# Kernel tuning notes

Measured on AMD Instinct MI355X. Metric: run time of the kernel, lower is better.

The kernel has to match this reference:

```python
import jax, jax.numpy as jnp
import numpy as np

D_MODEL, H, DK, DV = 1024, 16, 64, 64
B, NQ, NK = 4, 1024, 1024
LN_EPS = 1e-5


def setup_inputs() -> dict:
    key = jax.random.key(0)
    ks = jax.random.split(key, 16)
    xavier = lambda k, i, o: jax.random.uniform(k, (i, o), jnp.float32,
                                                -np.sqrt(6.0 / (i + o)), np.sqrt(6.0 / (i + o)))
    return {
        "queries": jax.random.normal(ks[0], (B, NQ, D_MODEL), jnp.float32),
        "keys": jax.random.normal(ks[1], (B, NK, D_MODEL), jnp.float32),
        "values": jax.random.normal(ks[2], (B, NK, D_MODEL), jnp.float32),
        "geometry": jax.random.uniform(ks[3], (B, H, NQ, NK), jnp.float32),
        "attention_mask": jax.random.bernoulli(ks[4], 0.1, (B, H, NQ, NK)),
        "Wq": xavier(ks[5], D_MODEL, H * DK), "bq": jnp.zeros((H * DK,), jnp.float32),
        "Wk": xavier(ks[6], D_MODEL, H * DK), "bk": jnp.zeros((H * DK,), jnp.float32),
        "Wv": xavier(ks[7], D_MODEL, H * DV), "bv": jnp.zeros((H * DV,), jnp.float32),
        "Wo": xavier(ks[8], H * DV, D_MODEL), "bo": jnp.zeros((D_MODEL,), jnp.float32),
        "ln_gamma": jnp.ones((D_MODEL,), jnp.float32),
        "ln_beta": jnp.zeros((D_MODEL,), jnp.float32),
    }


def reference(queries, keys, values, geometry, attention_mask,
              Wq, bq, Wk, bk, Wv, bv, Wo, bo, ln_gamma, ln_beta):
    b, nq, _ = queries.shape
    nk = keys.shape[1]
    # QKV projections -> (b, h, n, d)
    q = (queries @ Wq + bq).reshape(b, nq, H, DK).transpose(0, 2, 1, 3)
    k = (keys @ Wk + bk).reshape(b, nk, H, DK).transpose(0, 2, 1, 3)
    v = (values @ Wv + bv).reshape(b, nk, H, DV).transpose(0, 2, 1, 3)
    att = jnp.einsum('bhqd,bhkd->bhqk', q, k) / np.sqrt(DK).astype(np.float32)
    att = jnp.where(attention_mask, -jnp.inf, att)
    # inline geometry log-bias before softmax
    w = jnp.log(jnp.clip(geometry, 1e-6)) + att
    w = jax.nn.softmax(w, axis=-1)  # dropout is identity in eval
    out = jnp.einsum('bhqk,bhkd->bqhd', w, v).reshape(b, nq, H * DV)
    out = out @ Wo + bo
    # residual + LayerNorm
    x = queries + out  # dropout identity in eval
    mu = jnp.mean(x, axis=-1, keepdims=True)
    var = jnp.mean((x - mu) ** 2, axis=-1, keepdims=True)
    return (x - mu) * jax.lax.rsqrt(var + LN_EPS) * ln_gamma + ln_beta
```

## Files before the change

kernel.cpp:

```cpp
#include <hip/hip_runtime.h>
#include <hip/hip_bf16.h>

typedef unsigned short u16;
typedef unsigned char u8;
typedef unsigned long long u64;
typedef __bf16 bf16x8 __attribute__((ext_vector_type(8)));
typedef float f32x4 __attribute__((ext_vector_type(4)));

#define AS1 __attribute__((address_space(1)))
#define AS3 __attribute__((address_space(3)))
#define GLL16(gp, lp) __builtin_amdgcn_global_load_lds((AS1 const unsigned int*)(gp), (AS3 unsigned int*)(lp), 16, 0, 0)
#define NTL4(p) __builtin_nontemporal_load((const f32x4*)(p))

__device__ __forceinline__ u16 f2bf(float f) {
    unsigned u = __builtin_bit_cast(unsigned, f);
    unsigned r = u + 0x7FFFu + ((u >> 16) & 1u);
    return (u16)(r >> 16);
}

__global__ __launch_bounds__(256) void prep_kernel(
    const float* __restrict__ q, const float* __restrict__ k, const float* __restrict__ v,
    u16* __restrict__ xq, u16* __restrict__ xk, u16* __restrict__ xv,
    const float* __restrict__ W0, const float* __restrict__ W1,
    const float* __restrict__ W2, const float* __restrict__ W3,
    u16* __restrict__ T0, u16* __restrict__ T1, u16* __restrict__ T2, u16* __restrict__ T3) {
    const int gb = blockIdx.x, tid = threadIdx.x;
    if (gb < 1024) {
        const int n4 = 4 * 1024 * 1024 / 4;
        const int stride = 1024 * 256;
        for (int i = gb * 256 + tid; i < n4; i += stride) {
            float4 a = ((const float4*)q)[i];
            float4 b = ((const float4*)k)[i];
            float4 c = ((const float4*)v)[i];
            ((ushort4*)xq)[i] = make_ushort4(f2bf(a.x), f2bf(a.y), f2bf(a.z), f2bf(a.w));
            ((ushort4*)xk)[i] = make_ushort4(f2bf(b.x), f2bf(b.y), f2bf(b.z), f2bf(b.w));
            ((ushort4*)xv)[i] = make_ushort4(f2bf(c.x), f2bf(c.y), f2bf(c.z), f2bf(c.w));
        }
    } else {
        __shared__ float t[64][65];
        const int idx = gb - 1024;
        const int bz = idx >> 8, by = (idx >> 4) & 15, bx = idx & 15;
        const float* W = (bz == 0) ? W0 : (bz == 1) ? W1 : (bz == 2) ? W2 : W3;
        u16* T = (bz == 0) ? T0 : (bz == 1) ? T1 : (bz == 2) ? T2 : T3;
        const int n0 = bx * 64, k0 = by * 64;
        const int tx = tid & 63, ty = tid >> 6;
        for (int j = ty; j < 64; j += 4) t[j][tx] = W[(size_t)(k0 + j) * 1024 + n0 + tx];
        __syncthreads();
        for (int j = ty; j < 64; j += 4) T[(size_t)(n0 + j) * 1024 + k0 + tx] = f2bf(t[tx][j]);
    }
}

#define MN_LOOP(PRED)                                                     \
    for (int row = wave; row < 65536; row += nw) {                        \
        size_t base = (size_t)row * 1024;                                 \
        u64 myw = 0;                                                      \
        _Pragma("unroll")                                                 \
        for (int kb = 0; kb < 16; ++kb) {                                 \
            size_t gi = base + kb * 64 + lane;                            \
            bool p = (PRED);                                              \
            u64 w = __ballot(p);                                          \
            if (lane == kb) myw = w;                                      \
        }                                                                 \
        if (lane < 16) MB[(size_t)row * 16 + lane] = myw;                 \
    }

__global__ __launch_bounds__(256) void masknorm_kernel(const void* __restrict__ mp,
                                                       u64* __restrict__ MB) {
    __shared__ int s_cnt1, s_big;
    if (threadIdx.x == 0) { s_cnt1 = 0; s_big = 0; }
    __syncthreads();
    {
        const unsigned char* m8 = (const unsigned char*)mp;
        int c1 = 0, bg = 0;
        for (int i = threadIdx.x; i < 16384; i += 256) {
            unsigned char vv = m8[i];
            if (vv) {
                if ((i & 3) == 1) c1++;
                if (vv > 1) bg++;
            }
        }
        atomicAdd(&s_cnt1, c1);
        atomicAdd(&s_big, bg);
    }
    __syncthreads();
    const int flag = (s_big == 0) ? (s_cnt1 ? 0 : 1) : (s_cnt1 ? 3 : 2);

    const int lane = threadIdx.x & 63;
    const int wave = blockIdx.x * 4 + (threadIdx.x >> 6);
    const int nw = gridDim.x * 4;
    if (flag == 0) {
        const unsigned char* m8 = (const unsigned char*)mp;
        MN_LOOP(m8[gi] != 0)
    } else if (flag == 1) {
        const int* m32 = (const int*)mp;
        MN_LOOP(m32[gi] != 0)
    } else if (flag == 2) {
        const unsigned* mf = (const unsigned*)mp;
        MN_LOOP((mf[gi] << 1) != 0)
    } else {
        const u16* mb = (const u16*)mp;
        MN_LOOP((mb[gi] & 0x7FFF) != 0)
    }
}

__device__ __forceinline__ void gemm_core(const u16* __restrict__ A, const u16* __restrict__ Bt,
                                          u16* sA, u16* sB, f32x4 (&acc)[4][4],
                                          int tid, int bm, int bn) {
    const int lane = tid & 63, wid = tid >> 6;
    const int wr = wid >> 1, wc = wid & 1;
    const int l15 = lane & 15, l4 = lane >> 4;
    const int srow = tid >> 2, sslot = tid & 3;
    const int soff = (sslot ^ ((srow >> 1) & 3)) * 8;
    const u16* aSrc = A + (size_t)(bm * 128 + srow) * 1024 + soff;
    const u16* bSrc = Bt + (size_t)(bn * 128 + srow) * 1024 + soff;
    u16* const dA0 = sA + wid * 512;
    u16* const dA1 = sA + 2048 + wid * 512;
    u16* const dB0 = sB + wid * 512;
    u16* const dB1 = sB + 2048 + wid * 512;

#define GSTAGE(BUF, T)                                                  \
    do {                                                                \
        GLL16(aSrc + (T) * 32, dA0 + (BUF) * 4096);                     \
        GLL16(aSrc + 65536 + (T) * 32, dA1 + (BUF) * 4096);             \
        GLL16(bSrc + (T) * 32, dB0 + (BUF) * 4096);                     \
        GLL16(bSrc + 65536 + (T) * 32, dB1 + (BUF) * 4096);             \
    } while (0)

#define GCOMPUTE(BUF)                                                             \
    do {                                                                          \
        bf16x8 af[4], bfv[4];                                                     \
        _Pragma("unroll")                                                         \
        for (int m = 0; m < 4; ++m) {                                             \
            const int rr = wr * 64 + m * 16 + l15;                                \
            af[m] = *(const bf16x8*)(sA + (BUF) * 4096 + rr * 32 +                \
                                     ((l4 ^ ((rr >> 1) & 3)) * 8));               \
        }                                                                         \
        _Pragma("unroll")                                                         \
        for (int n = 0; n < 4; ++n) {                                             \
            const int rr = wc * 64 + n * 16 + l15;                                \
            bfv[n] = *(const bf16x8*)(sB + (BUF) * 4096 + rr * 32 +               \
                                      ((l4 ^ ((rr >> 1) & 3)) * 8));              \
        }                                                                         \
        _Pragma("unroll")                                                         \
        for (int m = 0; m < 4; ++m)                                               \
            _Pragma("unroll")                                                     \
            for (int n = 0; n < 4; ++n)                                           \
                acc[m][n] = __builtin_amdgcn_mfma_f32_16x16x32_bf16(af[m], bfv[n], acc[m][n], 0, 0, 0); \
    } while (0)

#define GBODY(T, BUF, NBUF, WSTR)                                       \
    do {                                                                \
        if ((T) + 2 < 32) {                                             \
            GSTAGE(NBUF, (T) + 2);                                      \
            __builtin_amdgcn_sched_barrier(0);                          \
        }                                                               \
        GCOMPUTE(BUF);                                                  \
        if ((T) + 1 < 32) {                                             \
            asm volatile(WSTR ::: "memory");                            \
            __builtin_amdgcn_sched_barrier(0);                          \
            __builtin_amdgcn_s_barrier();                               \
            __builtin_amdgcn_sched_barrier(0);                          \
        }                                                               \
    } while (0)

    GSTAGE(0, 0);
    GSTAGE(1, 1);
    __builtin_amdgcn_sched_barrier(0);
    asm volatile("s_waitcnt vmcnt(4)" ::: "memory");
    __builtin_amdgcn_sched_barrier(0);
    __builtin_amdgcn_s_barrier();
    __builtin_amdgcn_sched_barrier(0);

    for (int it = 0; it < 10; ++it) {
        const int t0 = it * 3;
        GBODY(t0 + 0, 0, 2, "s_waitcnt vmcnt(4)");
        GBODY(t0 + 1, 1, 0, "s_waitcnt vmcnt(4)");
        GBODY(t0 + 2, 2, 1, "s_waitcnt vmcnt(4)");
    }
    GBODY(30, 0, 2, "s_waitcnt vmcnt(0)");
    GBODY(31, 1, 0, "s_waitcnt vmcnt(0)");
#undef GBODY
#undef GCOMPUTE
#undef GSTAGE
}

__global__ __launch_bounds__(256, 3) void qkv_gemm(
    const u16* __restrict__ XQ, const u16* __restrict__ XK, const u16* __restrict__ XV,
    const u16* __restrict__ WQT, const u16* __restrict__ WKT, const u16* __restrict__ WVT,
    const float* __restrict__ bq, const float* __restrict__ bk, const float* __restrict__ bv,
    u16* __restrict__ QS, u16* __restrict__ KS, u16* __restrict__ VT) {
    __shared__ __align__(16) u16 smem[24576];
    const int z = blockIdx.z;
    const u16* A  = (z == 0) ? XQ : (z == 1) ? XK : XV;
    const u16* Bt = (z == 0) ? WQT : (z == 1) ? WKT : WVT;
    const float* bias = (z == 0) ? bq : (z == 1) ? bk : bv;
    const int tid = threadIdx.x, lane = tid & 63, wid = tid >> 6;
    const int bm = blockIdx.x * 4 + (blockIdx.y >> 3);
    const int bn = blockIdx.y & 7;
    const int wr = wid >> 1, wc = wid & 1;
    const int l15 = lane & 15, l4 = lane >> 4;

    f32x4 acc[4][4] = {};
    gemm_core(A, Bt, smem, smem + 12288, acc, tid, bm, bn);

    if (z == 2) {
        __syncthreads();
        u16* tl = smem;
#pragma unroll
        for (int n = 0; n < 4; ++n) {
            const int cl = wc * 64 + n * 16 + l15;
            const float bv_ = bias[bn * 128 + cl];
#pragma unroll
            for (int m = 0; m < 4; ++m)
#pragma unroll
                for (int j = 0; j < 4; ++j) {
                    const int rl = wr * 64 + m * 16 + l4 * 4 + j;
                    tl[cl * 132 + rl] = f2bf(acc[m][n][j] + bv_);
                }
        }
        __syncthreads();
        const int bb = bm >> 3, k0 = (bm & 7) * 128;
#pragma unroll
        for (int i = 0; i < 8; ++i) {
            const int idx = i * 256 + tid;
            const int row = idx >> 4, col16 = idx & 15;
            const int cg = bn * 128 + row;
            const int hh = cg >> 6, dd = cg & 63;
            bf16x8 v = *(const bf16x8*)(tl + row * 132 + col16 * 8);
            *(bf16x8*)(VT + ((size_t)((bb * 16 + hh) * 64 + dd)) * 1024 + k0 + col16 * 8) = v;
        }
    } else {
        u16* outp = (z == 0) ? QS : KS;
        const float scale = (z == 0) ? 0.125f : 1.0f;
#pragma unroll
        for (int n = 0; n < 4; ++n) {
            const int c = bn * 128 + wc * 64 + n * 16 + l15;
            const float bv_ = bias[c];
#pragma unroll
            for (int m = 0; m < 4; ++m)
#pragma unroll
                for (int j = 0; j < 4; ++j) {
                    const int r = bm * 128 + wr * 64 + m * 16 + l4 * 4 + j;
                    outp[(size_t)r * 1024 + c] = f2bf((acc[m][n][j] + bv_) * scale);
                }
        }
    }
}

__global__ __launch_bounds__(256, 3) void gemm_out(
    const u16* __restrict__ A, const u16* __restrict__ Bt, const float* __restrict__ bias,
    float* __restrict__ outp, const float* __restrict__ resid) {
    __shared__ __align__(16) u16 smem[24576];
    const int tid = threadIdx.x, lane = tid & 63, wid = tid >> 6;
    const int bm = blockIdx.x * 4 + (blockIdx.y >> 3);
    const int bn = blockIdx.y & 7;
    const int wr = wid >> 1, wc = wid & 1;
    const int l15 = lane & 15, l4 = lane >> 4;

    f32x4 acc[4][4] = {};
    gemm_core(A, Bt, smem, smem + 12288, acc, tid, bm, bn);

#pragma unroll
    for (int n = 0; n < 4; ++n) {
        const int c = bn * 128 + wc * 64 + n * 16 + l15;
        const float bv = bias[c];
#pragma unroll
        for (int m = 0; m < 4; ++m)
#pragma unroll
            for (int j = 0; j < 4; ++j) {
                const int r = bm * 128 + wr * 64 + m * 16 + l4 * 4 + j;
                outp[(size_t)r * 1024 + c] = acc[m][n][j] + bv + resid[(size_t)r * 1024 + c];
            }
    }
}

__global__ __launch_bounds__(256, 3) void attn_kernel(
    const u16* __restrict__ Qs, const u16* __restrict__ Ks, const u16* __restrict__ Vt,
    const float* __restrict__ geom, const u64* __restrict__ MBw,
    u16* __restrict__ AO) {
    __shared__ __align__(16) u16 lds[20480];

    const int g = blockIdx.x;
    const int tt = (g & 7) * 128 + (g >> 3);
    const int qb = tt & 15;
    const int bhid = tt >> 4;
    const int b = bhid >> 4, h = bhid & 15;
    const int q0 = qb * 64;

    const int tid = threadIdx.x, lane = tid & 63, wid = tid >> 6;
    const int l15 = lane & 15, l4 = lane >> 4;
    const int qrow = q0 + wid * 16;
    const size_t bh = (size_t)bhid;

    const u16* qp = Qs + (size_t)(b * 1024 + qrow + l15) * 1024 + h * 64 + l4 * 8;
    bf16x8 aq0 = *(const bf16x8*)qp;
    bf16x8 aq1 = *(const bf16x8*)(qp + 32);

    const int r0 = tid >> 3, s0 = tid & 7;
    const int r1 = 32 + r0;
    const int kgr0 = (r0 & 15) * 4 + (r0 >> 4);
    const int kgr1 = (r1 & 15) * 4 + (r1 >> 4);
    const u16* ksrc0 = Ks + (size_t)(b * 1024 + kgr0) * 1024 + h * 64 + ((s0 ^ (r0 & 7)) * 8);
    const u16* ksrc1 = Ks + (size_t)(b * 1024 + kgr1) * 1024 + h * 64 + ((s0 ^ (r1 & 7)) * 8);
    const u16* vsrc0 = Vt + (bh * 64 + r0) * 1024 + ((s0 ^ (r0 & 7)) * 8);
    const u16* vsrc1 = Vt + (bh * 64 + r1) * 1024 + ((s0 ^ (r1 & 7)) * 8);
    u16* const KD = lds + wid * 512;
    u16* const VD = lds + 8192 + wid * 512;
    u16* const pw = lds + 16384 + wid * 1024;

    const float* gbase = geom + (bh * 1024 + qrow + l4 * 4) * 1024 + l15 * 4;
    const u8* mbase8 = (const u8*)MBw + (size_t)(bh * 1024 + qrow + l4 * 4) * 128 + (l15 >> 1);
    const int nsh = (l15 & 1) * 4;

    f32x4 o[4] = {};
    float m_run[4], l_run[4];
#pragma unroll
    for (int j = 0; j < 4; ++j) { m_run[j] = -1e30f; l_run[j] = 0.f; }

    f32x4 gpA[4], gpB[4];
    unsigned mkA[4], mkB[4];

    GLL16(ksrc0, KD);
    GLL16(ksrc1, KD + 2048);
    GLL16(vsrc0, VD);
    GLL16(vsrc1, VD + 2048);
    __builtin_amdgcn_sched_barrier(0);
#pragma unroll
    for (int j = 0; j < 4; ++j) {
        gpA[j] = NTL4(gbase + j * 1024);
        mkA[j] = __builtin_nontemporal_load(mbase8 + j * 128);
    }
    __builtin_amdgcn_sched_barrier(0);
    asm volatile("s_waitcnt vmcnt(8)" ::: "memory");
    __builtin_amdgcn_sched_barrier(0);
    __builtin_amdgcn_s_barrier();
    __builtin_amdgcn_sched_barrier(0);

#define BODY(T, G, GC, GN, MC, MN)                                                       \
    do {                                                                                 \
        const u16* KB = lds + ((T) & 1) * 4096;                                          \
        const u16* VB = lds + 8192 + ((T) & 1) * 4096;                                   \
        if (G) {                                                                         \
            const int nb = (((T) + 1) & 1) * 4096;                                       \
            GLL16(ksrc0 + (size_t)((T) + 1) * 65536, KD + nb);                           \
            GLL16(ksrc1 + (size_t)((T) + 1) * 65536, KD + 2048 + nb);                    \
            GLL16(vsrc0 + ((T) + 1) * 64, VD + nb);                                      \
            GLL16(vsrc1 + ((T) + 1) * 64, VD + 2048 + nb);                               \
            __builtin_amdgcn_sched_barrier(0);                                           \
            _Pragma("unroll")                                                            \
            for (int j = 0; j < 4; ++j) {                                                \
                GN[j] = NTL4(gbase + j * 1024 + ((T) + 1) * 64);                         \
                MN[j] = __builtin_nontemporal_load(mbase8 + j * 128 + ((T) + 1) * 8);    \
            }                                                                            \
            __builtin_amdgcn_sched_barrier(0);                                           \
        }                                                                                \
        f32x4 s[4];                                                                      \
        __builtin_amdgcn_s_setprio(1);                                                   \
        _Pragma("unroll")                                                                \
        for (int nf = 0; nf < 4; ++nf) {                                                 \
            const int rr = nf * 16 + l15, swz = rr & 7;                                  \
            bf16x8 k0 = *(const bf16x8*)(KB + rr * 64 + ((l4 ^ swz) * 8));               \
            bf16x8 k1 = *(const bf16x8*)(KB + rr * 64 + (((4 + l4) ^ swz) * 8));         \
            f32x4 z = {};                                                                \
            z = __builtin_amdgcn_mfma_f32_16x16x32_bf16(aq0, k0, z, 0, 0, 0);            \
            s[nf] = __builtin_amdgcn_mfma_f32_16x16x32_bf16(aq1, k1, z, 0, 0, 0);        \
        }                                                                                \
        __builtin_amdgcn_s_setprio(0);                                                   \
        float sclv[4];                                                                   \
        _Pragma("unroll")                                                                \
        for (int j = 0; j < 4; ++j) {                                                    \
            float mt = fmaxf(fmaxf(s[0][j], s[1][j]), fmaxf(s[2][j], s[3][j]));          \
            mt = fmaxf(mt, __shfl_xor(mt, 1, 16));                                       \
            mt = fmaxf(mt, __shfl_xor(mt, 2, 16));                                       \
            mt = fmaxf(mt, __shfl_xor(mt, 4, 16));                                       \
            mt = fmaxf(mt, __shfl_xor(mt, 8, 16));                                       \
            float mn = fmaxf(m_run[j], mt);                                              \
            float scl = __expf(m_run[j] - mn);                                           \
            m_run[j] = mn;                                                               \
            unsigned nib = (MC[j] >> nsh) & 0xFu;                                        \
            f32x4 gv = GC[j];                                                            \
            float p0 = (nib & 1u) ? 0.f : __expf(s[0][j] - mn) * fmaxf(gv[0], 1e-6f);    \
            float p1 = (nib & 2u) ? 0.f : __expf(s[1][j] - mn) * fmaxf(gv[1], 1e-6f);    \
            float p2 = (nib & 4u) ? 0.f : __expf(s[2][j] - mn) * fmaxf(gv[2], 1e-6f);    \
            float p3 = (nib & 8u) ? 0.f : __expf(s[3][j] - mn) * fmaxf(gv[3], 1e-6f);    \
            float rs = (p0 + p1) + (p2 + p3);                                            \
            rs += __shfl_xor(rs, 1, 16);                                                 \
            rs += __shfl_xor(rs, 2, 16);                                                 \
            rs += __shfl_xor(rs, 4, 16);                                                 \
            rs += __shfl_xor(rs, 8, 16);                                                 \
            l_run[j] = l_run[j] * scl + rs;                                              \
            sclv[j] = scl;                                                               \
            const int row = l4 * 4 + j;                                                  \
            u64 pk = (u64)f2bf(p0) | ((u64)f2bf(p1) << 16) |                             \
                     ((u64)f2bf(p2) << 32) | ((u64)f2bf(p3) << 48);                      \
            *(u64*)(pw + row * 64 + (((l15 >> 1) ^ (row & 7)) * 8) + (l15 & 1) * 4) = pk;\
        }                                                                                \
        _Pragma("unroll")                                                                \
        for (int df = 0; df < 4; ++df) {                                                 \
            f32x4 tv = o[df];                                                            \
            _Pragma("unroll")                                                            \
            for (int j = 0; j < 4; ++j) tv[j] *= sclv[j];                                \
            o[df] = tv;                                                                  \
        }                                                                                \
        {                                                                                \
            const int pswz = l15 & 7;                                                    \
            bf16x8 pa0 = *(const bf16x8*)(pw + l15 * 64 + ((l4 ^ pswz) * 8));            \
            bf16x8 pa1 = *(const bf16x8*)(pw + l15 * 64 + (((4 + l4) ^ pswz) * 8));      \
            __builtin_amdgcn_s_setprio(1);                                               \
            _Pragma("unroll")                                                            \
            for (int df = 0; df < 4; ++df) {                                             \
                const int rr = df * 16 + l15, vswz = rr & 7;                             \
                bf16x8 v0 = *(const bf16x8*)(VB + rr * 64 + ((l4 ^ vswz) * 8));          \
                bf16x8 v1 = *(const bf16x8*)(VB + rr * 64 + (((4 + l4) ^ vswz) * 8));    \
                o[df] = __builtin_amdgcn_mfma_f32_16x16x32_bf16(pa0, v0, o[df], 0, 0, 0);\
                o[df] = __builtin_amdgcn_mfma_f32_16x16x32_bf16(pa1, v1, o[df], 0, 0, 0);\
            }                                                                            \
            __builtin_amdgcn_s_setprio(0);                                               \
        }                                                                                \
        if (G) {                                                                         \
            asm volatile("s_waitcnt vmcnt(8)" ::: "memory");                             \
            __builtin_amdgcn_sched_barrier(0);                                           \
            __builtin_amdgcn_s_barrier();                                                \
            __builtin_amdgcn_sched_barrier(0);                                           \
        }                                                                                \
    } while (0)

    for (int it = 0; it < 7; ++it) {
        const int t0 = it * 2;
        BODY(t0,     1, gpA, gpB, mkA, mkB);
        BODY(t0 + 1, 1, gpB, gpA, mkB, mkA);
    }
    BODY(14, 1, gpA, gpB, mkA, mkB);
    BODY(15, 0, gpB, gpA, mkB, mkA);
#undef BODY

    float inv[4];
#pragma unroll
    for (int j = 0; j < 4; ++j) inv[j] = 1.0f / l_run[j];
#pragma unroll
    for (int df = 0; df < 4; ++df)
#pragma unroll
        for (int j = 0; j < 4; ++j)
            pw[(l4 * 4 + j) * 64 + df * 16 + l15] = f2bf(o[df][j] * inv[j]);
#pragma unroll
    for (int p = 0; p < 2; ++p) {
        const int idx = p * 64 + lane;
        const int er = idx >> 3, ec = idx & 7;
        bf16x8 val = *(const bf16x8*)(pw + er * 64 + ec * 8);
        *(bf16x8*)(AO + (size_t)(b * 1024 + qrow + er) * 1024 + h * 64 + ec * 8) = val;
    }
}

__global__ __launch_bounds__(256) void ln_kernel(const float* __restrict__ Y,
                                                 const float* __restrict__ gamma,
                                                 const float* __restrict__ beta,
                                                 float* __restrict__ out) {
    __shared__ float red[8];
    const int r = blockIdx.x, tid = threadIdx.x, lane = tid & 63, wid = tid >> 6;
    float4 v = ((const float4*)(Y + (size_t)r * 1024))[tid];
    float s = v.x + v.y + v.z + v.w;
    float q = v.x * v.x + v.y * v.y + v.z * v.z + v.w * v.w;
    for (int d = 1; d < 64; d <<= 1) {
        s += __shfl_xor(s, d, 64);
        q += __shfl_xor(q, d, 64);
    }
    if (lane == 0) { red[wid] = s; red[4 + wid] = q; }
    __syncthreads();
    float ts = red[0] + red[1] + red[2] + red[3];
    float tq = red[4] + red[5] + red[6] + red[7];
    float mu = ts * (1.f / 1024.f);
    float var = tq * (1.f / 1024.f) - mu * mu;
    float rstd = rsqrtf(var + 1e-5f);
    float4 gg = ((const float4*)gamma)[tid];
    float4 be = ((const float4*)beta)[tid];
    float4 ov;
    ov.x = (v.x - mu) * rstd * gg.x + be.x;
    ov.y = (v.y - mu) * rstd * gg.y + be.y;
    ov.z = (v.z - mu) * rstd * gg.z + be.z;
    ov.w = (v.w - mu) * rstd * gg.w + be.w;
    ((float4*)(out + (size_t)r * 1024))[tid] = ov;
}

extern "C" void kernel_launch(void* const* d_in, const int* in_sizes, int n_in,
                              void* d_out, int out_size, void* d_ws, size_t ws_size,
                              hipStream_t stream) {
    const float* queries = (const float*)d_in[0];
    const float* keys    = (const float*)d_in[1];
    const float* values  = (const float*)d_in[2];
    const float* geom    = (const float*)d_in[3];
    const void*  mask    = d_in[4];
    const float* Wq = (const float*)d_in[5];  const float* bq = (const float*)d_in[6];
    const float* Wk = (const float*)d_in[7];  const float* bk = (const float*)d_in[8];
    const float* Wv = (const float*)d_in[9];  const float* bv = (const float*)d_in[10];
    const float* Wo = (const float*)d_in[11]; const float* bo = (const float*)d_in[12];
    const float* gamma = (const float*)d_in[13];
    const float* beta  = (const float*)d_in[14];

    char* ws = (char*)d_ws;
    const size_t MB_ = 1024 * 1024;
    u16* XQ  = (u16*)(ws + 0);
    u16* XK  = (u16*)(ws + 8 * MB_);
    u16* XV  = (u16*)(ws + 16 * MB_);
    u16* WQT = (u16*)(ws + 24 * MB_);
    u16* WKT = (u16*)(ws + 26 * MB_);
    u16* WVT = (u16*)(ws + 28 * MB_);
    u16* WOT = (u16*)(ws + 30 * MB_);
    u16* QS  = (u16*)(ws + 32 * MB_);
    u16* KS  = (u16*)(ws + 40 * MB_);
    u16* VT  = (u16*)(ws + 48 * MB_);
    u16* AO  = (u16*)(ws + 56 * MB_);
    u64* MBITS = (u64*)(ws + 16 * MB_);
    float* Y = (float*)(ws + 0);

    prep_kernel<<<2048, 256, 0, stream>>>(queries, keys, values, XQ, XK, XV,
                                          Wq, Wk, Wv, Wo, WQT, WKT, WVT, WOT);
    qkv_gemm<<<dim3(8, 32, 3), 256, 0, stream>>>(XQ, XK, XV, WQT, WKT, WVT, bq, bk, bv, QS, KS, VT);
    masknorm_kernel<<<1024, 256, 0, stream>>>(mask, MBITS);
    attn_kernel<<<1024, 256, 0, stream>>>(QS, KS, VT, geom, MBITS, AO);
    gemm_out<<<dim3(8, 32), 256, 0, stream>>>(AO, WOT, bo, Y, queries);
    ln_kernel<<<4096, 256, 0, stream>>>(Y, gamma, beta, (float*)d_out);
}
```

Before: 260.9 us.

## Fuse fp32-to-bf16 activation conversion into QKV GEMM A-tile loading

The separate pass that converted queries, keys and values from fp32 to bf16 in the workspace is removed. The QKV GEMM now reads fp32 activations straight into registers, converts them to bf16 and writes swizzled tiles to LDS, while the weight tiles still stream in through global_load_lds. This avoids writing and re-reading 24 MB of bf16 intermediates. In exchange the GEMM reads twice as many A bytes, each block re-converts its A tiles once per N-block, and the register-staged A path adds VGPR pressure and a software pipeline with manual waitcnt bookkeeping.

```diff
diff --git a/kernel.cpp b/kernel.cpp
--- a/kernel.cpp
+++ b/kernel.cpp
@@ -19,35 +19,19 @@
 }
 
 __global__ __launch_bounds__(256) void prep_kernel(
-    const float* __restrict__ q, const float* __restrict__ k, const float* __restrict__ v,
-    u16* __restrict__ xq, u16* __restrict__ xk, u16* __restrict__ xv,
     const float* __restrict__ W0, const float* __restrict__ W1,
     const float* __restrict__ W2, const float* __restrict__ W3,
     u16* __restrict__ T0, u16* __restrict__ T1, u16* __restrict__ T2, u16* __restrict__ T3) {
-    const int gb = blockIdx.x, tid = threadIdx.x;
-    if (gb < 1024) {
-        const int n4 = 4 * 1024 * 1024 / 4;
-        const int stride = 1024 * 256;
-        for (int i = gb * 256 + tid; i < n4; i += stride) {
-            float4 a = ((const float4*)q)[i];
-            float4 b = ((const float4*)k)[i];
-            float4 c = ((const float4*)v)[i];
-            ((ushort4*)xq)[i] = make_ushort4(f2bf(a.x), f2bf(a.y), f2bf(a.z), f2bf(a.w));
-            ((ushort4*)xk)[i] = make_ushort4(f2bf(b.x), f2bf(b.y), f2bf(b.z), f2bf(b.w));
-            ((ushort4*)xv)[i] = make_ushort4(f2bf(c.x), f2bf(c.y), f2bf(c.z), f2bf(c.w));
-        }
-    } else {
-        __shared__ float t[64][65];
-        const int idx = gb - 1024;
-        const int bz = idx >> 8, by = (idx >> 4) & 15, bx = idx & 15;
-        const float* W = (bz == 0) ? W0 : (bz == 1) ? W1 : (bz == 2) ? W2 : W3;
-        u16* T = (bz == 0) ? T0 : (bz == 1) ? T1 : (bz == 2) ? T2 : T3;
-        const int n0 = bx * 64, k0 = by * 64;
-        const int tx = tid & 63, ty = tid >> 6;
-        for (int j = ty; j < 64; j += 4) t[j][tx] = W[(size_t)(k0 + j) * 1024 + n0 + tx];
-        __syncthreads();
-        for (int j = ty; j < 64; j += 4) T[(size_t)(n0 + j) * 1024 + k0 + tx] = f2bf(t[tx][j]);
-    }
+    __shared__ float t[64][65];
+    const int idx = blockIdx.x, tid = threadIdx.x;
+    const int bz = idx >> 8, by = (idx >> 4) & 15, bx = idx & 15;
+    const float* W = (bz == 0) ? W0 : (bz == 1) ? W1 : (bz == 2) ? W2 : W3;
+    u16* T = (bz == 0) ? T0 : (bz == 1) ? T1 : (bz == 2) ? T2 : T3;
+    const int n0 = bx * 64, k0 = by * 64;
+    const int tx = tid & 63, ty = tid >> 6;
+    for (int j = ty; j < 64; j += 4) t[j][tx] = W[(size_t)(k0 + j) * 1024 + n0 + tx];
+    __syncthreads();
+    for (int j = ty; j < 64; j += 4) T[(size_t)(n0 + j) * 1024 + k0 + tx] = f2bf(t[tx][j]);
 }
 
 #define MN_LOOP(PRED)                                                     \
@@ -180,18 +164,115 @@
     GBODY(30, 0, 2, "s_waitcnt vmcnt(0)");
     GBODY(31, 1, 0, "s_waitcnt vmcnt(0)");
 #undef GBODY
+#undef GSTAGE
+}
+
+__device__ __forceinline__ void gemm_core_f32a(const float* __restrict__ Af, const u16* __restrict__ Bt,
+                                               u16* sA, u16* sB, f32x4 (&acc)[4][4],
+                                               int tid, int bm, int bn) {
+    const int lane = tid & 63, wid = tid >> 6;
+    const int wr = wid >> 1, wc = wid & 1;
+    const int l15 = lane & 15, l4 = lane >> 4;
+    const int srow = tid >> 2, sslot = tid & 3;
+    const int soff = (sslot ^ ((srow >> 1) & 3)) * 8;
+    const u16* bSrc = Bt + (size_t)(bn * 128 + srow) * 1024 + soff;
+    u16* const dB0 = sB + wid * 512;
+    u16* const dB1 = sB + 2048 + wid * 512;
+    const int arow = tid >> 1, ah = tid & 1;
+    const float* aSrcF = Af + (size_t)(bm * 128 + arow) * 1024 + ah * 16;
+    const int aswz = (arow >> 1) & 3;
+    u16* const aW0 = sA + arow * 32 + (((ah * 2) ^ aswz) * 8);
+    u16* const aW1 = sA + arow * 32 + (((ah * 2 + 1) ^ aswz) * 8);
+
+    f32x4 rA[4], rB[4];
+
+#define BSTAGE(BUF, T)                                                  \
+    do {                                                                \
+        GLL16(bSrc + (T) * 32, dB0 + (BUF) * 4096);                     \
+        GLL16(bSrc + 65536 + (T) * 32, dB1 + (BUF) * 4096);             \
+    } while (0)
+
+#define ALOAD(AR, T)                                                    \
+    do {                                                                \
+        AR[0] = *(const f32x4*)(aSrcF + (T) * 32);                      \
+        AR[1] = *(const f32x4*)(aSrcF + (T) * 32 + 4);                  \
+        AR[2] = *(const f32x4*)(aSrcF + (T) * 32 + 8);                  \
+        AR[3] = *(const f32x4*)(aSrcF + (T) * 32 + 12);                 \
+    } while (0)
+
+#define ASTORE(MBUF, AR)                                                \
+    do {                                                                \
+        bf16x8 w0, w1;                                                  \
+        _Pragma("unroll")                                               \
+        for (int j = 0; j < 4; ++j) {                                   \
+            w0[j] = (__bf16)AR[0][j];                                   \
+            w0[4 + j] = (__bf16)AR[1][j];                               \
+            w1[j] = (__bf16)AR[2][j];                                   \
+            w1[4 + j] = (__bf16)AR[3][j];                               \
+        }                                                               \
+        *(bf16x8*)(aW0 + (MBUF) * 4096) = w0;                           \
+        *(bf16x8*)(aW1 + (MBUF) * 4096) = w1;                           \
+    } while (0)
+
+#define FBODY(T, BUF, MBUF, NBUF, ACUR, ANXT, WSTR)                     \
+    do {                                                                \
+        if ((T) + 2 < 32) {                                             \
+            BSTAGE(NBUF, (T) + 2);                                      \
+            __builtin_amdgcn_sched_barrier(0);                          \
+            ALOAD(ANXT, (T) + 2);                                       \
+            __builtin_amdgcn_sched_barrier(0);                          \
+        }                                                               \
+        GCOMPUTE(BUF);                                                  \
+        if ((T) + 1 < 32) {                                             \
+            asm volatile(WSTR ::: "memory");                            \
+            __builtin_amdgcn_sched_barrier(0);                          \
+            ASTORE(MBUF, ACUR);                                         \
+            asm volatile("s_waitcnt lgkmcnt(0)" ::: "memory");          \
+            __builtin_amdgcn_sched_barrier(0);                          \
+            __builtin_amdgcn_s_barrier();                               \
+            __builtin_amdgcn_sched_barrier(0);                          \
+        }                                                               \
+    } while (0)
+
+    BSTAGE(0, 0);
+    ALOAD(rA, 0);
+    BSTAGE(1, 1);
+    ALOAD(rB, 1);
+    __builtin_amdgcn_sched_barrier(0);
+    asm volatile("s_waitcnt vmcnt(6)" ::: "memory");
+    __builtin_amdgcn_sched_barrier(0);
+    ASTORE(0, rA);
+    asm volatile("s_waitcnt lgkmcnt(0)" ::: "memory");
+    __builtin_amdgcn_sched_barrier(0);
+    __builtin_amdgcn_s_barrier();
+    __builtin_amdgcn_sched_barrier(0);
+
+    for (int it = 0; it < 5; ++it) {
+        const int t0 = it * 6;
+        FBODY(t0 + 0, 0, 1, 2, rB, rA, "s_waitcnt vmcnt(6)");
+        FBODY(t0 + 1, 1, 2, 0, rA, rB, "s_waitcnt vmcnt(6)");
+        FBODY(t0 + 2, 2, 0, 1, rB, rA, "s_waitcnt vmcnt(6)");
+        FBODY(t0 + 3, 0, 1, 2, rA, rB, "s_waitcnt vmcnt(6)");
+        FBODY(t0 + 4, 1, 2, 0, rB, rA, "s_waitcnt vmcnt(6)");
+        FBODY(t0 + 5, 2, 0, 1, rA, rB, "s_waitcnt vmcnt(6)");
+    }
+    FBODY(30, 0, 1, 2, rB, rA, "s_waitcnt vmcnt(0)");
+    FBODY(31, 1, 2, 0, rA, rB, "s_waitcnt vmcnt(0)");
+#undef FBODY
+#undef ASTORE
+#undef ALOAD
+#undef BSTAGE
 #undef GCOMPUTE
-#undef GSTAGE
 }
 
 __global__ __launch_bounds__(256, 3) void qkv_gemm(
-    const u16* __restrict__ XQ, const u16* __restrict__ XK, const u16* __restrict__ XV,
+    const float* __restrict__ Qf, const float* __restrict__ Kf, const float* __restrict__ Vf,
     const u16* __restrict__ WQT, const u16* __restrict__ WKT, const u16* __restrict__ WVT,
     const float* __restrict__ bq, const float* __restrict__ bk, const float* __restrict__ bv,
     u16* __restrict__ QS, u16* __restrict__ KS, u16* __restrict__ VT) {
     __shared__ __align__(16) u16 smem[24576];
     const int z = blockIdx.z;
-    const u16* A  = (z == 0) ? XQ : (z == 1) ? XK : XV;
+    const float* A = (z == 0) ? Qf : (z == 1) ? Kf : Vf;
     const u16* Bt = (z == 0) ? WQT : (z == 1) ? WKT : WVT;
     const float* bias = (z == 0) ? bq : (z == 1) ? bk : bv;
     const int tid = threadIdx.x, lane = tid & 63, wid = tid >> 6;
@@ -201,7 +282,7 @@
     const int l15 = lane & 15, l4 = lane >> 4;
 
     f32x4 acc[4][4] = {};
-    gemm_core(A, Bt, smem, smem + 12288, acc, tid, bm, bn);
+    gemm_core_f32a(A, Bt, smem, smem + 12288, acc, tid, bm, bn);
 
     if (z == 2) {
         __syncthreads();
@@ -498,9 +579,6 @@
 
     char* ws = (char*)d_ws;
     const size_t MB_ = 1024 * 1024;
-    u16* XQ  = (u16*)(ws + 0);
-    u16* XK  = (u16*)(ws + 8 * MB_);
-    u16* XV  = (u16*)(ws + 16 * MB_);
     u16* WQT = (u16*)(ws + 24 * MB_);
     u16* WKT = (u16*)(ws + 26 * MB_);
     u16* WVT = (u16*)(ws + 28 * MB_);
@@ -512,9 +590,9 @@
     u64* MBITS = (u64*)(ws + 16 * MB_);
     float* Y = (float*)(ws + 0);
 
-    prep_kernel<<<2048, 256, 0, stream>>>(queries, keys, values, XQ, XK, XV,
-                                          Wq, Wk, Wv, Wo, WQT, WKT, WVT, WOT);
-    qkv_gemm<<<dim3(8, 32, 3), 256, 0, stream>>>(XQ, XK, XV, WQT, WKT, WVT, bq, bk, bv, QS, KS, VT);
+    prep_kernel<<<1024, 256, 0, stream>>>(Wq, Wk, Wv, Wo, WQT, WKT, WVT, WOT);
+    qkv_gemm<<<dim3(8, 32, 3), 256, 0, stream>>>(queries, keys, values, WQT, WKT, WVT,
+                                                 bq, bk, bv, QS, KS, VT);
     masknorm_kernel<<<1024, 256, 0, stream>>>(mask, MBITS);
     attn_kernel<<<1024, 256, 0, stream>>>(QS, KS, VT, geom, MBITS, AO);
     gemm_out<<<dim3(8, 32), 256, 0, stream>>>(AO, WOT, bo, Y, queries);
```

Measured after the change: 268.0 us. 1.03x slower.
